# Kernel tuning notes

Hardware: AMD Instinct MI355X
Metric: run time of the kernel (lower is better)

The kernel has to match this reference:

```python
import jax, jax.numpy as jnp
import numpy as np

CUTOFF = 3.0   # self.cutoff
RMIN = 3.5     # rmin in cutoff_function (note rmin > cutoff, faithful to source)
ETA = 4.0
N_RADIAL = 5
N_3BODY = 12
NATOMS = 2048
K = 48         # neighbors per atom (equal counts -> ragged loop becomes dense batch)
HID = 64
NPAIRS = NATOMS * K


def setup_inputs() -> dict:
    key = jax.random.key(0)
    ks = jax.random.split(key, 4)
    # displacements scaled so |rij| is mostly within a few Angstrom
    rij = jax.random.normal(ks[0], (NPAIRS, 3), jnp.float32) * 1.5
    # sorted-by-atom pair list with K neighbors per atom
    unique_i = jnp.repeat(jnp.arange(NATOMS, dtype=jnp.int64), K)
    W1 = jax.random.normal(ks[1], (N_RADIAL + N_3BODY, HID), jnp.float32) * 0.1
    b1 = jnp.zeros((HID,), jnp.float32)
    W2 = jax.random.normal(ks[2], (HID, HID), jnp.float32) * 0.1
    b2 = jnp.zeros((HID,), jnp.float32)
    W3 = jax.random.normal(ks[3], (HID, 1), jnp.float32) * 0.1
    b3 = jnp.zeros((1,), jnp.float32)
    return dict(rij=rij, unique_i=unique_i, W1=W1, b1=b1, W2=W2, b2=b2, W3=W3, b3=b3)


def _energy(rij, W1, b1, W2, b2, W3, b3):
    d = jnp.linalg.norm(rij, axis=1, keepdims=True)           # (P,1)
    diff_norm = rij / jnp.maximum(d, 1e-12)                   # F.normalize
    # pair cutoff (rmin=3.5, c=3.0 as in source)
    fc = jnp.where(d > RMIN,
                   0.5 + 0.5 * jnp.cos(jnp.pi * (d - RMIN) / (CUTOFF - RMIN)),
                   1.0)
    # radial Bessel basis, n = 1..5
    ns = jnp.arange(1, N_RADIAL + 1, dtype=rij.dtype)
    rbf = jnp.sqrt(2.0 / CUTOFF) * jnp.sin(ns * jnp.pi / CUTOFF * d) / d * fc  # (P,5)
    # 3-body Gaussian descriptors
    fcrik = (0.5 + 0.5 * jnp.cos(jnp.pi * d / CUTOFF))[:, 0]  # (P,)
    dn = diff_norm.reshape(NATOMS, K, 3)
    cosang = jnp.einsum('nkd,nld->nkl', dn, dn)               # (N,K,K) pairwise mm
    cosang = jnp.where(jnp.eye(K, dtype=bool)[None], 0.0, cosang)  # fill_diagonal_(0)
    mu = jnp.linspace(-1.0, 1.0, N_3BODY).astype(rij.dtype)
    w = fcrik.reshape(NATOMS, 1, K, 1)                        # fcrik broadcast on axis being summed
    g3b = jnp.sum(jnp.exp(-ETA * (cosang[..., None] - mu) ** 2) * w, axis=2)  # (N,K,12)
    g3b = g3b.reshape(NPAIRS, N_3BODY)
    desc = jnp.concatenate([rbf, g3b], axis=1)                # (P,17)
    h = jnp.tanh(desc @ W1 + b1)
    h = jnp.tanh(h @ W2 + b2)
    eij = h @ W3 + b3                                         # (P,1)
    return jnp.sum(eij * fc)


def reference(rij, unique_i, W1, b1, W2, b2, W3, b3):
    # Module output: gradients of total energy w.r.t. rij (written into beta)
    return jax.grad(_energy)(rij, W1, b1, W2, b2, W3, b3)
```

## Files before the change

kernel.cpp:

```cpp
#include <hip/hip_runtime.h>
#include <hip/hip_bf16.h>

#define NATOMS 2048
#define K 48
#define NR 5
#define NM 12
#define ND 17
#define HID 64

#define PI_F 3.14159265358979f
#define CUT 3.0f
#define RMIN_F 3.5f
#define AFC (-6.28318530717959f)
#define POC (PI_F / CUT)
#define SQ 0.816496580927726f
#define CMC (-0.132231404958678f)
#define N4L (-5.77078016355585f)
#define E1L (2.09846551402031f)
#define TL2 (2.88539008177793f)

__device__ unsigned short g_w1t[64 * 32];
__device__ unsigned short g_w2t[64 * 64];
__device__ unsigned short g_w2r[64 * 64];
__device__ unsigned short g_w1r[32 * 64];

using frag_ab = __attribute__((ext_vector_type(8))) short;
using frag_cd = __attribute__((ext_vector_type(4))) float;
using f2 = __attribute__((ext_vector_type(2))) float;
using f4 = __attribute__((ext_vector_type(4))) float;
using s4 = __attribute__((ext_vector_type(4))) short;

__device__ __forceinline__ float fast_tanh(float x) {
    const float t = __builtin_amdgcn_exp2f(TL2 * x);
    return 1.0f - 2.0f * __builtin_amdgcn_rcpf(t + 1.0f);
}

__device__ __forceinline__ unsigned short f2bs(float x) {
    __hip_bfloat16 b = __float2bfloat16(x);
    return __builtin_bit_cast(unsigned short, b);
}

__device__ __forceinline__ float bs2f(unsigned short u) {
    return __builtin_bit_cast(float, ((unsigned)u) << 16);
}

template <int CTRL>
__device__ __forceinline__ float dpp_add(float x) {
    const int y = __builtin_amdgcn_update_dpp(
        0, __builtin_bit_cast(int, x), CTRL, 0xF, 0xF, true);
    return x + __builtin_bit_cast(float, y);
}

__global__ __launch_bounds__(256) void k_prep(const float* __restrict__ W1,
                                              const float* __restrict__ W2) {
    const int i = blockIdx.x * 256 + threadIdx.x;
    if (i < 2048) {
        const int n = i >> 5, k = i & 31;
        g_w1t[i] = (k < ND) ? f2bs(W1[k * HID + n]) : (unsigned short)0;
    } else if (i < 2048 + 4096) {
        const int j = i - 2048, n = j >> 6, k = j & 63;
        g_w2t[j] = f2bs(W2[k * HID + n]);
    } else if (i < 2048 + 8192) {
        const int j = i - (2048 + 4096);
        g_w2r[j] = f2bs(W2[j]);
    } else if (i < 2048 + 8192 + 2048) {
        const int j = i - (2048 + 8192), n = j >> 6;
        g_w1r[j] = (n < ND) ? f2bs(W1[j]) : (unsigned short)0;
    }
}

#define H1_OFF   0
#define TT_OFF   0
#define SST_OFF  4992
#define GZ2_OFF  6912
#define DESC_OFF 13824
#define SGD_OFF  13824
#define SU_OFF   17664
#define SFC_OFF  18432
#define SFK_OFF  18624
#define SM_BYTES 18816

__global__ __launch_bounds__(64, 2) void k_fused(const float* __restrict__ rij,
                                                 const float* __restrict__ b1,
                                                 const float* __restrict__ b2,
                                                 const float* __restrict__ W3,
                                                 const float* __restrict__ b3,
                                                 float* __restrict__ out) {
    __shared__ __align__(16) char smem[SM_BYTES];
    short*          h1S   = (short*)(smem + H1_OFF);
    unsigned short* tT    = (unsigned short*)(smem + TT_OFF);
    unsigned short* tS    = (unsigned short*)(smem + SST_OFF);
    short*          gz2S  = (short*)(smem + GZ2_OFF);
    short*          descS = (short*)(smem + DESC_OFF);
    float*          sgd   = (float*)(smem + SGD_OFF);
    float*          su    = (float*)(smem + SU_OFF);
    float*          sfc   = (float*)(smem + SFC_OFF);
    float*          sfk   = (float*)(smem + SFK_OFF);

    const int lane = threadIdx.x;
    const int quad = lane >> 4, lm = lane & 15;
    const int base3 = blockIdx.x * (K * 3);

    float b1v[4], b2v[4], w3v[4];
#pragma unroll
    for (int nt = 0; nt < 4; nt++) {
        b1v[nt] = b1[nt * 16 + lm];
        b2v[nt] = b2[nt * 16 + lm];
        w3v[nt] = W3[nt * 16 + lm];
    }
    const float b3v = b3[0];

    if (lane < K) {
        const float x = rij[base3 + 3 * lane];
        const float y = rij[base3 + 3 * lane + 1];
        const float z = rij[base3 + 3 * lane + 2];
        float s2 = fmaxf(x * x + y * y + z * z, 1e-24f);
        const float inv = __builtin_amdgcn_rsqf(s2);
        const float d = s2 * inv;
        *(f4*)&su[4 * lane] = (f4){x * inv, y * inv, z * inv, d};
        sfk[lane] = 0.5f + 0.5f * __cosf(POC * d);
        const float fc = (d > RMIN_F) ? (0.5f + 0.5f * __cosf(AFC * (d - RMIN_F))) : 1.0f;
        sfc[lane] = fc;
        float s1, c1;
        __sincosf(POC * d, &s1, &c1);
        const float sc = SQ * fc * inv;
        float sn = s1, cn = c1;
#pragma unroll 1
        for (int n = 0; n < NR; n++) {
            descS[lane * 40 + n] = (short)f2bs(sc * sn);
            const float snx = sn * c1 + cn * s1;
            cn = cn * c1 - sn * s1;
            sn = snx;
        }
#pragma unroll 1
        for (int c = ND; c < 32; c++) descS[lane * 40 + c] = 0;
    }

    if (lane < K) {
        const int k = lane;
        const f4 uk = *(const f4*)&su[4 * k];
        f2 partv[6];
#pragma unroll
        for (int i = 0; i < 6; i++) partv[i] = (f2){0.0f, 0.0f};
#pragma unroll 1
        for (int l = 0; l < K; l++) {
            const f4 ul = *(const f4*)&su[4 * l];
            float c = uk.x * ul.x + uk.y * ul.y + uk.z * ul.z;
            if (k == l) c = 0.0f;
            const float cp1 = c + 1.0f;
            const float e0 = __builtin_amdgcn_exp2f(N4L * cp1 * cp1) * sfk[l];
            const float e1 = __builtin_amdgcn_exp2f(E1L * cp1);
            const float e2s = e1 * e1;
            const f2 e2v = {e2s, e2s};
            f2 tm = {e0, e0 * e1};
            partv[0] += tm;
#pragma unroll
            for (int i = 1; i < 6; i++) { tm *= e2v; partv[i] += tm; }
        }
#pragma unroll
        for (int i = 0; i < 6; i++) {
            const int m0 = 2 * i, m1 = 2 * i + 1;
            descS[k * 40 + NR + m0] = (short)f2bs(partv[i].x * __expf(CMC * (float)(m0 * m0)));
            descS[k * 40 + NR + m1] = (short)f2bs(partv[i].y * __expf(CMC * (float)(m1 * m1)));
        }
    }

    {
        frag_ab wf1[4];
#pragma unroll
        for (int nt = 0; nt < 4; nt++)
            wf1[nt] = *(const frag_ab*)&g_w1t[(nt * 16 + lm) * 32 + quad * 8];
#pragma unroll 1
        for (int mt = 0; mt < 3; mt++) {
            const frag_ab a = *(const frag_ab*)&descS[(mt * 16 + lm) * 40 + quad * 8];
#pragma unroll
            for (int nt = 0; nt < 4; nt++) {
                frag_cd acc = {b1v[nt], b1v[nt], b1v[nt], b1v[nt]};
                acc = __builtin_amdgcn_mfma_f32_16x16x32_bf16(a, wf1[nt], acc, 0, 0, 0);
#pragma unroll
                for (int r = 0; r < 4; r++)
                    h1S[(mt * 16 + quad * 4 + r) * 72 + nt * 16 + lm] =
                        (short)f2bs(fast_tanh(acc[r]));
            }
        }
    }

    {
        frag_ab wa[4], wb[4];
#pragma unroll
        for (int nt = 0; nt < 4; nt++) {
            wa[nt] = *(const frag_ab*)&g_w2t[(nt * 16 + lm) * 64 + quad * 8];
            wb[nt] = *(const frag_ab*)&g_w2t[(nt * 16 + lm) * 64 + 32 + quad * 8];
        }
#pragma unroll 1
        for (int mt = 0; mt < 3; mt++) {
            const frag_ab a0 = *(const frag_ab*)&h1S[(mt * 16 + lm) * 72 + quad * 8];
            const frag_ab a1 = *(const frag_ab*)&h1S[(mt * 16 + lm) * 72 + 32 + quad * 8];
            const f4 fcv = *(const f4*)&sfc[mt * 16 + quad * 4];
            float ep[4] = {0.0f, 0.0f, 0.0f, 0.0f};
#pragma unroll
            for (int nt = 0; nt < 4; nt++) {
                frag_cd acc = {b2v[nt], b2v[nt], b2v[nt], b2v[nt]};
                acc = __builtin_amdgcn_mfma_f32_16x16x32_bf16(a0, wa[nt], acc, 0, 0, 0);
                acc = __builtin_amdgcn_mfma_f32_16x16x32_bf16(a1, wb[nt], acc, 0, 0, 0);
#pragma unroll
                for (int r = 0; r < 4; r++) {
                    const int row = mt * 16 + quad * 4 + r;
                    const float tv = fast_tanh(acc[r]);
                    ep[r] = fmaf(tv, w3v[nt], ep[r]);
                    gz2S[row * 72 + nt * 16 + lm] =
                        (short)f2bs(fcv[r] * w3v[nt] * (1.0f - tv * tv));
                }
            }
#pragma unroll
            for (int r = 0; r < 4; r++)
                ep[r] = dpp_add<0x118>(dpp_add<0x114>(dpp_add<0x112>(dpp_add<0x111>(ep[r]))));
            if (lm == 15) {
#pragma unroll
                for (int r = 0; r < 4; r++)
                    sgd[(mt * 16 + quad * 4 + r) * 20 + 17] = ep[r] + b3v;
            }
        }
    }

    {
        frag_ab wa[4], wb[4];
#pragma unroll
        for (int nt = 0; nt < 4; nt++) {
            wa[nt] = *(const frag_ab*)&g_w2r[(nt * 16 + lm) * 64 + quad * 8];
            wb[nt] = *(const frag_ab*)&g_w2r[(nt * 16 + lm) * 64 + 32 + quad * 8];
        }
#pragma unroll 1
        for (int mt = 0; mt < 3; mt++) {
            const frag_ab a0 = *(const frag_ab*)&gz2S[(mt * 16 + lm) * 72 + quad * 8];
            const frag_ab a1 = *(const frag_ab*)&gz2S[(mt * 16 + lm) * 72 + 32 + quad * 8];
#pragma unroll
            for (int nt = 0; nt < 4; nt++) {
                frag_cd acc = {0.0f, 0.0f, 0.0f, 0.0f};
                acc = __builtin_amdgcn_mfma_f32_16x16x32_bf16(a0, wa[nt], acc, 0, 0, 0);
                acc = __builtin_amdgcn_mfma_f32_16x16x32_bf16(a1, wb[nt], acc, 0, 0, 0);
#pragma unroll
                for (int r = 0; r < 4; r++) {
                    const int idx = (mt * 16 + quad * 4 + r) * 72 + nt * 16 + lm;
                    const float tv = bs2f((unsigned short)h1S[idx]);
                    h1S[idx] = (short)f2bs(acc[r] * (1.0f - tv * tv));
                }
            }
        }
    }

    {
        frag_ab wa[2], wb[2];
#pragma unroll
        for (int nt = 0; nt < 2; nt++) {
            wa[nt] = *(const frag_ab*)&g_w1r[(nt * 16 + lm) * 64 + quad * 8];
            wb[nt] = *(const frag_ab*)&g_w1r[(nt * 16 + lm) * 64 + 32 + quad * 8];
        }
        const float cm0 = (lm >= NR)
            ? __expf(CMC * (float)((lm - NR) * (lm - NR))) : 1.0f;
        const float cm1 = __expf(-16.0f);
#pragma unroll 1
        for (int mt = 0; mt < 3; mt++) {
            const frag_ab a0 = *(const frag_ab*)&h1S[(mt * 16 + lm) * 72 + quad * 8];
            const frag_ab a1 = *(const frag_ab*)&h1S[(mt * 16 + lm) * 72 + 32 + quad * 8];
            {
                frag_cd acc = {0.0f, 0.0f, 0.0f, 0.0f};
                acc = __builtin_amdgcn_mfma_f32_16x16x32_bf16(a0, wa[0], acc, 0, 0, 0);
                acc = __builtin_amdgcn_mfma_f32_16x16x32_bf16(a1, wb[0], acc, 0, 0, 0);
#pragma unroll
                for (int r = 0; r < 4; r++)
                    sgd[(mt * 16 + quad * 4 + r) * 20 + lm] = acc[r] * cm0;
            }
            {
                frag_cd acc = {0.0f, 0.0f, 0.0f, 0.0f};
                acc = __builtin_amdgcn_mfma_f32_16x16x32_bf16(a0, wa[1], acc, 0, 0, 0);
                acc = __builtin_amdgcn_mfma_f32_16x16x32_bf16(a1, wb[1], acc, 0, 0, 0);
                if (lm == 0) {
#pragma unroll
                    for (int r = 0; r < 4; r++)
                        sgd[(mt * 16 + quad * 4 + r) * 20 + 16] = acc[r] * cm1;
                }
            }
        }
    }

    float gx1 = 0.0f, gy1 = 0.0f, gz1 = 0.0f;
    if (lane < K) {
        const int k = lane;
        f2 gm[NM];
#pragma unroll
        for (int m = 0; m < NM; m++) {
            const float g = sgd[k * 20 + NR + m];
            gm[m] = (f2){g, (float)m * g};
        }
        const f4 uk = *(const f4*)&su[4 * k];
#pragma unroll 1
        for (int l = 0; l < K; l++) {
            const f4 ul = *(const f4*)&su[4 * l];
            float c = uk.x * ul.x + uk.y * ul.y + uk.z * ul.z;
            if (k == l) c = 0.0f;
            const float cp1 = c + 1.0f;
            const float e0 = __builtin_amdgcn_exp2f(N4L * cp1 * cp1);
            const float x = __builtin_amdgcn_exp2f(E1L * cp1);
            const f2 xx = {x, x};
            f2 pd = gm[11];
#pragma unroll
            for (int m = 10; m >= 1; m--) pd = __builtin_elementwise_fma(pd, xx, gm[m]);
            const float Pv = fmaf(pd.x, x, gm[0].x);
            const float T = e0 * Pv;
            const float U = e0 * x * pd.y;
            const float Sp = fmaf(cp1, T, -(2.0f / 11.0f) * U);
            const float Sv = (k == l) ? 0.0f : (-8.0f) * Sp;
            tT[l * 52 + k] = f2bs(T);
            tS[l * 52 + k] = f2bs(Sv);
            const float A = Sv * sfk[l];
            gx1 = fmaf(A, ul.x, gx1);
            gy1 = fmaf(A, ul.y, gy1);
            gz1 = fmaf(A, ul.z, gz1);
        }
    }

    if (lane < K) {
        const int k = lane;
        float sgf_t = 0.0f, gx2 = 0.0f, gy2 = 0.0f, gz2v = 0.0f;
#pragma unroll 1
        for (int i = 0; i < 12; i++) {
            const s4 tv4 = *(const s4*)&tT[k * 52 + 4 * i];
            const s4 sv4 = *(const s4*)&tS[k * 52 + 4 * i];
#pragma unroll
            for (int j = 0; j < 4; j++) {
                const int l = 4 * i + j;
                const f4 ul = *(const f4*)&su[4 * l];
                sgf_t += bs2f((unsigned short)tv4[j]);
                const float Sv = bs2f((unsigned short)sv4[j]);
                gx2 = fmaf(Sv, ul.x, gx2);
                gy2 = fmaf(Sv, ul.y, gy2);
                gz2v = fmaf(Sv, ul.z, gz2v);
            }
        }
        const float fk = sfk[k];
        const float gux = gx1 + fk * gx2;
        const float guy = gy1 + fk * gy2;
        const float guz = gz1 + fk * gz2v;

        const f4 uv = *(const f4*)&su[4 * k];
        const float d = uv.w;
        const float ux = uv.x, uy = uv.y, uz = uv.z;
        const float invd = __builtin_amdgcn_rcpf(d);
        float gfc = sgd[k * 20 + 17];
        float gdR = 0.0f;
        float s1, c1;
        __sincosf(POC * d, &s1, &c1);
        float sn = s1, cn = c1, bn = POC;
#pragma unroll 1
        for (int n = 0; n < NR; n++) {
            const float g = sgd[k * 20 + n];
            gfc = fmaf(g, SQ * sn * invd, gfc);
            gdR = fmaf(g, SQ * (bn * cn - sn * invd) * invd, gdR);
            const float snx = sn * c1 + cn * s1;
            cn = cn * c1 - sn * s1;
            sn = snx;
            bn += POC;
        }
        const float fc = sfc[k];
        float dfc = 0.0f;
        if (d > RMIN_F) dfc = -0.5f * AFC * __sinf(AFC * (d - RMIN_F));
        const float dfcrik = -0.5f * POC * __sinf(POC * d);

        const float gd = fc * gdR + gfc * dfc + sgf_t * dfcrik;
        const float dot = gux * ux + guy * uy + guz * uz;

        out[base3 + 3 * k + 0] = fmaf(gd, ux, (gux - dot * ux) * invd);
        out[base3 + 3 * k + 1] = fmaf(gd, uy, (guy - dot * uy) * invd);
        out[base3 + 3 * k + 2] = fmaf(gd, uz, (guz - dot * uz) * invd);
    }
}

extern "C" void kernel_launch(void* const* d_in, const int* in_sizes, int n_in,
                              void* d_out, int out_size, void* d_ws, size_t ws_size,
                              hipStream_t stream) {
    (void)in_sizes; (void)n_in; (void)out_size; (void)d_ws; (void)ws_size;
    const float* rij = (const float*)d_in[0];
    const float* W1 = (const float*)d_in[2];
    const float* b1 = (const float*)d_in[3];
    const float* W2 = (const float*)d_in[4];
    const float* b2 = (const float*)d_in[5];
    const float* W3 = (const float*)d_in[6];
    const float* b3 = (const float*)d_in[7];
    float* out = (float*)d_out;

    k_prep<<<48, 256, 0, stream>>>(W1, W2);
    k_fused<<<NATOMS, 64, 0, stream>>>(rij, b1, b2, W3, b3, out);
}
```

Baseline: 94.57 us.

## Split each atom across three waves with 4-lane neighbor partitioning

The fused kernel goes from one 64-lane wave per atom to three waves (192 threads), each owning 16 neighbor rows. The pairwise angular loops are split over 4 lanes per row and combined with DPP reductions. The second angular pass now recomputes T and S from the l-side gradient coefficients instead of writing transposed bf16 tiles to shared memory, so shared memory shrinks and more blocks fit per CU. In exchange it repeats the exp and polynomial evaluation, and the early stages rely on wave-local ordering without barriers. That ordering looks fragile: the sgd reads for other rows depend on a single __syncthreads, and su/sfk are written by lanes <48 of every wave, which is redundant but consistent.

After: 100.3 us. 6.1% more time.

```diff
diff --git a/kernel.cpp b/kernel.cpp
--- a/kernel.cpp
+++ b/kernel.cpp
@@ -28,7 +28,6 @@
 using frag_cd = __attribute__((ext_vector_type(4))) float;
 using f2 = __attribute__((ext_vector_type(2))) float;
 using f4 = __attribute__((ext_vector_type(4))) float;
-using s4 = __attribute__((ext_vector_type(4))) short;
 
 __device__ __forceinline__ float fast_tanh(float x) {
     const float t = __builtin_amdgcn_exp2f(TL2 * x);
@@ -69,36 +68,30 @@
     }
 }
 
-#define H1_OFF   0
-#define TT_OFF   0
-#define SST_OFF  4992
-#define GZ2_OFF  6912
-#define DESC_OFF 13824
-#define SGD_OFF  13824
-#define SU_OFF   17664
-#define SFC_OFF  18432
-#define SFK_OFF  18624
-#define SM_BYTES 18816
-
-__global__ __launch_bounds__(64, 2) void k_fused(const float* __restrict__ rij,
-                                                 const float* __restrict__ b1,
-                                                 const float* __restrict__ b2,
-                                                 const float* __restrict__ W3,
-                                                 const float* __restrict__ b3,
-                                                 float* __restrict__ out) {
+#define XS       72
+#define X_OFF    0
+#define SGD_OFF  6912
+#define SU_OFF   10752
+#define SFC_OFF  11520
+#define SFK_OFF  11712
+#define SM_BYTES 11904
+
+__global__ __launch_bounds__(192, 6) void k_fused(const float* __restrict__ rij,
+                                                  const float* __restrict__ b1,
+                                                  const float* __restrict__ b2,
+                                                  const float* __restrict__ W3,
+                                                  const float* __restrict__ b3,
+                                                  float* __restrict__ out) {
     __shared__ __align__(16) char smem[SM_BYTES];
-    short*          h1S   = (short*)(smem + H1_OFF);
-    unsigned short* tT    = (unsigned short*)(smem + TT_OFF);
-    unsigned short* tS    = (unsigned short*)(smem + SST_OFF);
-    short*          gz2S  = (short*)(smem + GZ2_OFF);
-    short*          descS = (short*)(smem + DESC_OFF);
-    float*          sgd   = (float*)(smem + SGD_OFF);
-    float*          su    = (float*)(smem + SU_OFF);
-    float*          sfc   = (float*)(smem + SFC_OFF);
-    float*          sfk   = (float*)(smem + SFK_OFF);
-
-    const int lane = threadIdx.x;
-    const int quad = lane >> 4, lm = lane & 15;
+    short* X   = (short*)(smem + X_OFF);
+    float* sgd = (float*)(smem + SGD_OFF);
+    float* su  = (float*)(smem + SU_OFF);
+    float* sfc = (float*)(smem + SFC_OFF);
+    float* sfk = (float*)(smem + SFK_OFF);
+
+    const int t = threadIdx.x;
+    const int w = t >> 6, lane = t & 63, quad = lane >> 4, lm = lane & 15;
+    const int row0 = 16 * w;
     const int base3 = blockIdx.x * (K * 3);
 
     float b1v[4], b2v[4], w3v[4];
@@ -121,32 +114,36 @@
         sfk[lane] = 0.5f + 0.5f * __cosf(POC * d);
         const float fc = (d > RMIN_F) ? (0.5f + 0.5f * __cosf(AFC * (d - RMIN_F))) : 1.0f;
         sfc[lane] = fc;
-        float s1, c1;
-        __sincosf(POC * d, &s1, &c1);
-        const float sc = SQ * fc * inv;
-        float sn = s1, cn = c1;
-#pragma unroll 1
-        for (int n = 0; n < NR; n++) {
-            descS[lane * 40 + n] = (short)f2bs(sc * sn);
-            const float snx = sn * c1 + cn * s1;
-            cn = cn * c1 - sn * s1;
-            sn = snx;
-        }
-#pragma unroll 1
-        for (int c = ND; c < 32; c++) descS[lane * 40 + c] = 0;
-    }
-
-    if (lane < K) {
-        const int k = lane;
-        const f4 uk = *(const f4*)&su[4 * k];
+        if ((lane >> 4) == w) {
+            float s1, c1;
+            __sincosf(POC * d, &s1, &c1);
+            const float sc = SQ * fc * inv;
+            float sn = s1, cn = c1;
+#pragma unroll 1
+            for (int n = 0; n < NR; n++) {
+                X[lane * XS + n] = (short)f2bs(sc * sn);
+                const float snx = sn * c1 + cn * s1;
+                cn = cn * c1 - sn * s1;
+                sn = snx;
+            }
+#pragma unroll 1
+            for (int c = ND; c < 32; c++) X[lane * XS + c] = 0;
+        }
+    }
+
+    const int r16 = lane >> 2, ch = lane & 3;
+    const int kk = row0 + r16;
+    const f4 ukk = *(const f4*)&su[4 * kk];
+    {
         f2 partv[6];
 #pragma unroll
         for (int i = 0; i < 6; i++) partv[i] = (f2){0.0f, 0.0f};
 #pragma unroll 1
-        for (int l = 0; l < K; l++) {
+        for (int li = 0; li < 12; li++) {
+            const int l = ch * 12 + li;
             const f4 ul = *(const f4*)&su[4 * l];
-            float c = uk.x * ul.x + uk.y * ul.y + uk.z * ul.z;
-            if (k == l) c = 0.0f;
+            float c = ukk.x * ul.x + ukk.y * ul.y + ukk.z * ul.z;
+            if (kk == l) c = 0.0f;
             const float cp1 = c + 1.0f;
             const float e0 = __builtin_amdgcn_exp2f(N4L * cp1 * cp1) * sfk[l];
             const float e1 = __builtin_amdgcn_exp2f(E1L * cp1);
@@ -159,160 +156,145 @@
         }
 #pragma unroll
         for (int i = 0; i < 6; i++) {
-            const int m0 = 2 * i, m1 = 2 * i + 1;
-            descS[k * 40 + NR + m0] = (short)f2bs(partv[i].x * __expf(CMC * (float)(m0 * m0)));
-            descS[k * 40 + NR + m1] = (short)f2bs(partv[i].y * __expf(CMC * (float)(m1 * m1)));
-        }
-    }
-
-    {
-        frag_ab wf1[4];
-#pragma unroll
-        for (int nt = 0; nt < 4; nt++)
-            wf1[nt] = *(const frag_ab*)&g_w1t[(nt * 16 + lm) * 32 + quad * 8];
-#pragma unroll 1
-        for (int mt = 0; mt < 3; mt++) {
-            const frag_ab a = *(const frag_ab*)&descS[(mt * 16 + lm) * 40 + quad * 8];
-#pragma unroll
-            for (int nt = 0; nt < 4; nt++) {
-                frag_cd acc = {b1v[nt], b1v[nt], b1v[nt], b1v[nt]};
-                acc = __builtin_amdgcn_mfma_f32_16x16x32_bf16(a, wf1[nt], acc, 0, 0, 0);
+            partv[i].x = dpp_add<0x4E>(dpp_add<0xB1>(partv[i].x));
+            partv[i].y = dpp_add<0x4E>(dpp_add<0xB1>(partv[i].y));
+        }
+        if (ch == 0) {
+#pragma unroll
+            for (int i = 0; i < 6; i++) {
+                const int m0 = 2 * i, m1 = 2 * i + 1;
+                X[kk * XS + NR + m0] = (short)f2bs(partv[i].x * __expf(CMC * (float)(m0 * m0)));
+                X[kk * XS + NR + m1] = (short)f2bs(partv[i].y * __expf(CMC * (float)(m1 * m1)));
+            }
+        }
+    }
+
+    float t1v[4][4];
+    {
+        const frag_ab a = *(const frag_ab*)&X[(row0 + lm) * XS + quad * 8];
+#pragma unroll
+        for (int nt = 0; nt < 4; nt++) {
+            const frag_ab bfr = *(const frag_ab*)&g_w1t[(nt * 16 + lm) * 32 + quad * 8];
+            frag_cd acc = {b1v[nt], b1v[nt], b1v[nt], b1v[nt]};
+            acc = __builtin_amdgcn_mfma_f32_16x16x32_bf16(a, bfr, acc, 0, 0, 0);
+#pragma unroll
+            for (int r = 0; r < 4; r++) {
+                const float tv = fast_tanh(acc[r]);
+                t1v[nt][r] = tv;
+                X[(row0 + quad * 4 + r) * XS + nt * 16 + lm] = (short)f2bs(tv);
+            }
+        }
+    }
+
+    {
+        const frag_ab a0 = *(const frag_ab*)&X[(row0 + lm) * XS + quad * 8];
+        const frag_ab a1 = *(const frag_ab*)&X[(row0 + lm) * XS + 32 + quad * 8];
+        const f4 fcv = *(const f4*)&sfc[row0 + quad * 4];
+        float ep[4] = {0.0f, 0.0f, 0.0f, 0.0f};
+#pragma unroll
+        for (int nt = 0; nt < 4; nt++) {
+            const frag_ab b0 = *(const frag_ab*)&g_w2t[(nt * 16 + lm) * 64 + quad * 8];
+            const frag_ab b1f = *(const frag_ab*)&g_w2t[(nt * 16 + lm) * 64 + 32 + quad * 8];
+            frag_cd acc = {b2v[nt], b2v[nt], b2v[nt], b2v[nt]};
+            acc = __builtin_amdgcn_mfma_f32_16x16x32_bf16(a0, b0, acc, 0, 0, 0);
+            acc = __builtin_amdgcn_mfma_f32_16x16x32_bf16(a1, b1f, acc, 0, 0, 0);
+#pragma unroll
+            for (int r = 0; r < 4; r++) {
+                const float tv = fast_tanh(acc[r]);
+                ep[r] = fmaf(tv, w3v[nt], ep[r]);
+                X[(row0 + quad * 4 + r) * XS + nt * 16 + lm] =
+                    (short)f2bs(fcv[r] * w3v[nt] * (1.0f - tv * tv));
+            }
+        }
+#pragma unroll
+        for (int r = 0; r < 4; r++)
+            ep[r] = dpp_add<0x118>(dpp_add<0x114>(dpp_add<0x112>(dpp_add<0x111>(ep[r]))));
+        if (lm == 15) {
+#pragma unroll
+            for (int r = 0; r < 4; r++)
+                sgd[(row0 + quad * 4 + r) * 20 + 5] = ep[r] + b3v;
+        }
+    }
+
+    {
+        const frag_ab a0 = *(const frag_ab*)&X[(row0 + lm) * XS + quad * 8];
+        const frag_ab a1 = *(const frag_ab*)&X[(row0 + lm) * XS + 32 + quad * 8];
+#pragma unroll
+        for (int nt = 0; nt < 4; nt++) {
+            const frag_ab b0 = *(const frag_ab*)&g_w2r[(nt * 16 + lm) * 64 + quad * 8];
+            const frag_ab b1f = *(const frag_ab*)&g_w2r[(nt * 16 + lm) * 64 + 32 + quad * 8];
+            frag_cd acc = {0.0f, 0.0f, 0.0f, 0.0f};
+            acc = __builtin_amdgcn_mfma_f32_16x16x32_bf16(a0, b0, acc, 0, 0, 0);
+            acc = __builtin_amdgcn_mfma_f32_16x16x32_bf16(a1, b1f, acc, 0, 0, 0);
+#pragma unroll
+            for (int r = 0; r < 4; r++) {
+                const float g = acc[r] * (1.0f - t1v[nt][r] * t1v[nt][r]);
+                X[(row0 + quad * 4 + r) * XS + nt * 16 + lm] = (short)f2bs(g);
+            }
+        }
+    }
+
+    {
+        const frag_ab a0 = *(const frag_ab*)&X[(row0 + lm) * XS + quad * 8];
+        const frag_ab a1 = *(const frag_ab*)&X[(row0 + lm) * XS + 32 + quad * 8];
+        {
+            const frag_ab b0 = *(const frag_ab*)&g_w1r[lm * 64 + quad * 8];
+            const frag_ab b1f = *(const frag_ab*)&g_w1r[lm * 64 + 32 + quad * 8];
+            frag_cd acc = {0.0f, 0.0f, 0.0f, 0.0f};
+            acc = __builtin_amdgcn_mfma_f32_16x16x32_bf16(a0, b0, acc, 0, 0, 0);
+            acc = __builtin_amdgcn_mfma_f32_16x16x32_bf16(a1, b1f, acc, 0, 0, 0);
+            const int col = (lm < NR) ? lm : lm + 3;
+            const int mm = lm - NR;
+            const float cm = (lm >= NR) ? __expf(CMC * (float)(mm * mm)) : 1.0f;
+#pragma unroll
+            for (int r = 0; r < 4; r++)
+                sgd[(row0 + quad * 4 + r) * 20 + col] = acc[r] * cm;
+        }
+        {
+            const frag_ab b0 = *(const frag_ab*)&g_w1r[(16 + lm) * 64 + quad * 8];
+            const frag_ab b1f = *(const frag_ab*)&g_w1r[(16 + lm) * 64 + 32 + quad * 8];
+            frag_cd acc = {0.0f, 0.0f, 0.0f, 0.0f};
+            acc = __builtin_amdgcn_mfma_f32_16x16x32_bf16(a0, b0, acc, 0, 0, 0);
+            acc = __builtin_amdgcn_mfma_f32_16x16x32_bf16(a1, b1f, acc, 0, 0, 0);
+            if (lm == 0) {
+                const float cm = __expf(-16.0f);
 #pragma unroll
                 for (int r = 0; r < 4; r++)
-                    h1S[(mt * 16 + quad * 4 + r) * 72 + nt * 16 + lm] =
-                        (short)f2bs(fast_tanh(acc[r]));
-            }
-        }
-    }
-
-    {
-        frag_ab wa[4], wb[4];
-#pragma unroll
-        for (int nt = 0; nt < 4; nt++) {
-            wa[nt] = *(const frag_ab*)&g_w2t[(nt * 16 + lm) * 64 + quad * 8];
-            wb[nt] = *(const frag_ab*)&g_w2t[(nt * 16 + lm) * 64 + 32 + quad * 8];
-        }
-#pragma unroll 1
-        for (int mt = 0; mt < 3; mt++) {
-            const frag_ab a0 = *(const frag_ab*)&h1S[(mt * 16 + lm) * 72 + quad * 8];
-            const frag_ab a1 = *(const frag_ab*)&h1S[(mt * 16 + lm) * 72 + 32 + quad * 8];
-            const f4 fcv = *(const f4*)&sfc[mt * 16 + quad * 4];
-            float ep[4] = {0.0f, 0.0f, 0.0f, 0.0f};
-#pragma unroll
-            for (int nt = 0; nt < 4; nt++) {
-                frag_cd acc = {b2v[nt], b2v[nt], b2v[nt], b2v[nt]};
-                acc = __builtin_amdgcn_mfma_f32_16x16x32_bf16(a0, wa[nt], acc, 0, 0, 0);
-                acc = __builtin_amdgcn_mfma_f32_16x16x32_bf16(a1, wb[nt], acc, 0, 0, 0);
-#pragma unroll
-                for (int r = 0; r < 4; r++) {
-                    const int row = mt * 16 + quad * 4 + r;
-                    const float tv = fast_tanh(acc[r]);
-                    ep[r] = fmaf(tv, w3v[nt], ep[r]);
-                    gz2S[row * 72 + nt * 16 + lm] =
-                        (short)f2bs(fcv[r] * w3v[nt] * (1.0f - tv * tv));
-                }
-            }
-#pragma unroll
-            for (int r = 0; r < 4; r++)
-                ep[r] = dpp_add<0x118>(dpp_add<0x114>(dpp_add<0x112>(dpp_add<0x111>(ep[r]))));
-            if (lm == 15) {
-#pragma unroll
-                for (int r = 0; r < 4; r++)
-                    sgd[(mt * 16 + quad * 4 + r) * 20 + 17] = ep[r] + b3v;
-            }
-        }
-    }
-
-    {
-        frag_ab wa[4], wb[4];
-#pragma unroll
-        for (int nt = 0; nt < 4; nt++) {
-            wa[nt] = *(const frag_ab*)&g_w2r[(nt * 16 + lm) * 64 + quad * 8];
-            wb[nt] = *(const frag_ab*)&g_w2r[(nt * 16 + lm) * 64 + 32 + quad * 8];
-        }
-#pragma unroll 1
-        for (int mt = 0; mt < 3; mt++) {
-            const frag_ab a0 = *(const frag_ab*)&gz2S[(mt * 16 + lm) * 72 + quad * 8];
-            const frag_ab a1 = *(const frag_ab*)&gz2S[(mt * 16 + lm) * 72 + 32 + quad * 8];
-#pragma unroll
-            for (int nt = 0; nt < 4; nt++) {
-                frag_cd acc = {0.0f, 0.0f, 0.0f, 0.0f};
-                acc = __builtin_amdgcn_mfma_f32_16x16x32_bf16(a0, wa[nt], acc, 0, 0, 0);
-                acc = __builtin_amdgcn_mfma_f32_16x16x32_bf16(a1, wb[nt], acc, 0, 0, 0);
-#pragma unroll
-                for (int r = 0; r < 4; r++) {
-                    const int idx = (mt * 16 + quad * 4 + r) * 72 + nt * 16 + lm;
-                    const float tv = bs2f((unsigned short)h1S[idx]);
-                    h1S[idx] = (short)f2bs(acc[r] * (1.0f - tv * tv));
-                }
-            }
-        }
-    }
-
-    {
-        frag_ab wa[2], wb[2];
-#pragma unroll
-        for (int nt = 0; nt < 2; nt++) {
-            wa[nt] = *(const frag_ab*)&g_w1r[(nt * 16 + lm) * 64 + quad * 8];
-            wb[nt] = *(const frag_ab*)&g_w1r[(nt * 16 + lm) * 64 + 32 + quad * 8];
-        }
-        const float cm0 = (lm >= NR)
-            ? __expf(CMC * (float)((lm - NR) * (lm - NR))) : 1.0f;
-        const float cm1 = __expf(-16.0f);
-#pragma unroll 1
-        for (int mt = 0; mt < 3; mt++) {
-            const frag_ab a0 = *(const frag_ab*)&h1S[(mt * 16 + lm) * 72 + quad * 8];
-            const frag_ab a1 = *(const frag_ab*)&h1S[(mt * 16 + lm) * 72 + 32 + quad * 8];
-            {
-                frag_cd acc = {0.0f, 0.0f, 0.0f, 0.0f};
-                acc = __builtin_amdgcn_mfma_f32_16x16x32_bf16(a0, wa[0], acc, 0, 0, 0);
-                acc = __builtin_amdgcn_mfma_f32_16x16x32_bf16(a1, wb[0], acc, 0, 0, 0);
-#pragma unroll
-                for (int r = 0; r < 4; r++)
-                    sgd[(mt * 16 + quad * 4 + r) * 20 + lm] = acc[r] * cm0;
-            }
-            {
-                frag_cd acc = {0.0f, 0.0f, 0.0f, 0.0f};
-                acc = __builtin_amdgcn_mfma_f32_16x16x32_bf16(a0, wa[1], acc, 0, 0, 0);
-                acc = __builtin_amdgcn_mfma_f32_16x16x32_bf16(a1, wb[1], acc, 0, 0, 0);
-                if (lm == 0) {
-#pragma unroll
-                    for (int r = 0; r < 4; r++)
-                        sgd[(mt * 16 + quad * 4 + r) * 20 + 16] = acc[r] * cm1;
-                }
+                    sgd[(row0 + quad * 4 + r) * 20 + 19] = acc[r] * cm;
             }
         }
     }
 
     float gx1 = 0.0f, gy1 = 0.0f, gz1 = 0.0f;
-    if (lane < K) {
-        const int k = lane;
-        f2 gm[NM];
-#pragma unroll
-        for (int m = 0; m < NM; m++) {
-            const float g = sgd[k * 20 + NR + m];
-            gm[m] = (f2){g, (float)m * g};
-        }
-        const f4 uk = *(const f4*)&su[4 * k];
-#pragma unroll 1
-        for (int l = 0; l < K; l++) {
+    {
+        const f4 gA = *(const f4*)&sgd[kk * 20 + 8];
+        const f4 gB = *(const f4*)&sgd[kk * 20 + 12];
+        const f4 gC = *(const f4*)&sgd[kk * 20 + 16];
+#pragma unroll 1
+        for (int li = 0; li < 12; li++) {
+            const int l = ch * 12 + li;
             const f4 ul = *(const f4*)&su[4 * l];
-            float c = uk.x * ul.x + uk.y * ul.y + uk.z * ul.z;
-            if (k == l) c = 0.0f;
+            float c = ukk.x * ul.x + ukk.y * ul.y + ukk.z * ul.z;
+            if (kk == l) c = 0.0f;
             const float cp1 = c + 1.0f;
             const float e0 = __builtin_amdgcn_exp2f(N4L * cp1 * cp1);
             const float x = __builtin_amdgcn_exp2f(E1L * cp1);
-            const f2 xx = {x, x};
-            f2 pd = gm[11];
-#pragma unroll
-            for (int m = 10; m >= 1; m--) pd = __builtin_elementwise_fma(pd, xx, gm[m]);
-            const float Pv = fmaf(pd.x, x, gm[0].x);
-            const float T = e0 * Pv;
-            const float U = e0 * x * pd.y;
+            float P = gC[3], Dd = 11.0f * gC[3];
+            P = fmaf(P, x, gC[2]); Dd = fmaf(Dd, x, 10.0f * gC[2]);
+            P = fmaf(P, x, gC[1]); Dd = fmaf(Dd, x, 9.0f * gC[1]);
+            P = fmaf(P, x, gC[0]); Dd = fmaf(Dd, x, 8.0f * gC[0]);
+            P = fmaf(P, x, gB[3]); Dd = fmaf(Dd, x, 7.0f * gB[3]);
+            P = fmaf(P, x, gB[2]); Dd = fmaf(Dd, x, 6.0f * gB[2]);
+            P = fmaf(P, x, gB[1]); Dd = fmaf(Dd, x, 5.0f * gB[1]);
+            P = fmaf(P, x, gB[0]); Dd = fmaf(Dd, x, 4.0f * gB[0]);
+            P = fmaf(P, x, gA[3]); Dd = fmaf(Dd, x, 3.0f * gA[3]);
+            P = fmaf(P, x, gA[2]); Dd = fmaf(Dd, x, 2.0f * gA[2]);
+            P = fmaf(P, x, gA[1]); Dd = fmaf(Dd, x, gA[1]);
+            P = fmaf(P, x, gA[0]);
+            const float T = e0 * P;
+            const float U = e0 * x * Dd;
             const float Sp = fmaf(cp1, T, -(2.0f / 11.0f) * U);
-            const float Sv = (k == l) ? 0.0f : (-8.0f) * Sp;
-            tT[l * 52 + k] = f2bs(T);
-            tS[l * 52 + k] = f2bs(Sv);
+            const float Sv = (kk == l) ? 0.0f : (-8.0f) * Sp;
             const float A = Sv * sfk[l];
             gx1 = fmaf(A, ul.x, gx1);
             gy1 = fmaf(A, ul.y, gy1);
@@ -320,59 +302,87 @@
         }
     }
 
-    if (lane < K) {
-        const int k = lane;
-        float sgf_t = 0.0f, gx2 = 0.0f, gy2 = 0.0f, gz2v = 0.0f;
-#pragma unroll 1
-        for (int i = 0; i < 12; i++) {
-            const s4 tv4 = *(const s4*)&tT[k * 52 + 4 * i];
-            const s4 sv4 = *(const s4*)&tS[k * 52 + 4 * i];
-#pragma unroll
-            for (int j = 0; j < 4; j++) {
-                const int l = 4 * i + j;
-                const f4 ul = *(const f4*)&su[4 * l];
-                sgf_t += bs2f((unsigned short)tv4[j]);
-                const float Sv = bs2f((unsigned short)sv4[j]);
-                gx2 = fmaf(Sv, ul.x, gx2);
-                gy2 = fmaf(Sv, ul.y, gy2);
-                gz2v = fmaf(Sv, ul.z, gz2v);
-            }
-        }
-        const float fk = sfk[k];
-        const float gux = gx1 + fk * gx2;
-        const float guy = gy1 + fk * gy2;
-        const float guz = gz1 + fk * gz2v;
-
-        const f4 uv = *(const f4*)&su[4 * k];
-        const float d = uv.w;
-        const float ux = uv.x, uy = uv.y, uz = uv.z;
-        const float invd = __builtin_amdgcn_rcpf(d);
-        float gfc = sgd[k * 20 + 17];
-        float gdR = 0.0f;
-        float s1, c1;
-        __sincosf(POC * d, &s1, &c1);
-        float sn = s1, cn = c1, bn = POC;
-#pragma unroll 1
-        for (int n = 0; n < NR; n++) {
-            const float g = sgd[k * 20 + n];
-            gfc = fmaf(g, SQ * sn * invd, gfc);
-            gdR = fmaf(g, SQ * (bn * cn - sn * invd) * invd, gdR);
-            const float snx = sn * c1 + cn * s1;
-            cn = cn * c1 - sn * s1;
-            sn = snx;
-            bn += POC;
-        }
-        const float fc = sfc[k];
-        float dfc = 0.0f;
-        if (d > RMIN_F) dfc = -0.5f * AFC * __sinf(AFC * (d - RMIN_F));
-        const float dfcrik = -0.5f * POC * __sinf(POC * d);
-
-        const float gd = fc * gdR + gfc * dfc + sgf_t * dfcrik;
-        const float dot = gux * ux + guy * uy + guz * uz;
-
-        out[base3 + 3 * k + 0] = fmaf(gd, ux, (gux - dot * ux) * invd);
-        out[base3 + 3 * k + 1] = fmaf(gd, uy, (guy - dot * uy) * invd);
-        out[base3 + 3 * k + 2] = fmaf(gd, uz, (guz - dot * uz) * invd);
+    __syncthreads();
+
+    {
+        float sgfp = 0.0f, gx2 = 0.0f, gy2 = 0.0f, gz2p = 0.0f;
+#pragma unroll 1
+        for (int li = 0; li < 12; li++) {
+            const int l = ch * 12 + li;
+            const f4 gA = *(const f4*)&sgd[l * 20 + 8];
+            const f4 gB = *(const f4*)&sgd[l * 20 + 12];
+            const f4 gC = *(const f4*)&sgd[l * 20 + 16];
+            const f4 ul = *(const f4*)&su[4 * l];
+            float c = ukk.x * ul.x + ukk.y * ul.y + ukk.z * ul.z;
+            if (kk == l) c = 0.0f;
+            const float cp1 = c + 1.0f;
+            const float e0 = __builtin_amdgcn_exp2f(N4L * cp1 * cp1);
+            const float x = __builtin_amdgcn_exp2f(E1L * cp1);
+            float P = gC[3], Dd = 11.0f * gC[3];
+            P = fmaf(P, x, gC[2]); Dd = fmaf(Dd, x, 10.0f * gC[2]);
+            P = fmaf(P, x, gC[1]); Dd = fmaf(Dd, x, 9.0f * gC[1]);
+            P = fmaf(P, x, gC[0]); Dd = fmaf(Dd, x, 8.0f * gC[0]);
+            P = fmaf(P, x, gB[3]); Dd = fmaf(Dd, x, 7.0f * gB[3]);
+            P = fmaf(P, x, gB[2]); Dd = fmaf(Dd, x, 6.0f * gB[2]);
+            P = fmaf(P, x, gB[1]); Dd = fmaf(Dd, x, 5.0f * gB[1]);
+            P = fmaf(P, x, gB[0]); Dd = fmaf(Dd, x, 4.0f * gB[0]);
+            P = fmaf(P, x, gA[3]); Dd = fmaf(Dd, x, 3.0f * gA[3]);
+            P = fmaf(P, x, gA[2]); Dd = fmaf(Dd, x, 2.0f * gA[2]);
+            P = fmaf(P, x, gA[1]); Dd = fmaf(Dd, x, gA[1]);
+            P = fmaf(P, x, gA[0]);
+            const float T = e0 * P;
+            const float U = e0 * x * Dd;
+            const float Sp = fmaf(cp1, T, -(2.0f / 11.0f) * U);
+            const float Sv = (kk == l) ? 0.0f : (-8.0f) * Sp;
+            sgfp += T;
+            gx2 = fmaf(Sv, ul.x, gx2);
+            gy2 = fmaf(Sv, ul.y, gy2);
+            gz2p = fmaf(Sv, ul.z, gz2p);
+        }
+        gx1 = dpp_add<0x4E>(dpp_add<0xB1>(gx1));
+        gy1 = dpp_add<0x4E>(dpp_add<0xB1>(gy1));
+        gz1 = dpp_add<0x4E>(dpp_add<0xB1>(gz1));
+        sgfp = dpp_add<0x4E>(dpp_add<0xB1>(sgfp));
+        gx2 = dpp_add<0x4E>(dpp_add<0xB1>(gx2));
+        gy2 = dpp_add<0x4E>(dpp_add<0xB1>(gy2));
+        gz2p = dpp_add<0x4E>(dpp_add<0xB1>(gz2p));
+
+        if (ch == 0) {
+            const float fk = sfk[kk];
+            const float gux = gx1 + fk * gx2;
+            const float guy = gy1 + fk * gy2;
+            const float guz = gz1 + fk * gz2p;
+
+            const float d = ukk.w;
+            const float ux = ukk.x, uy = ukk.y, uz = ukk.z;
+            const float invd = __builtin_amdgcn_rcpf(d);
+            float gfc = sgd[kk * 20 + 5];
+            float gdR = 0.0f;
+            float s1, c1;
+            __sincosf(POC * d, &s1, &c1);
+            float sn = s1, cn = c1, bn = POC;
+#pragma unroll 1
+            for (int n = 0; n < NR; n++) {
+                const float g = sgd[kk * 20 + n];
+                gfc = fmaf(g, SQ * sn * invd, gfc);
+                gdR = fmaf(g, SQ * (bn * cn - sn * invd) * invd, gdR);
+                const float snx = sn * c1 + cn * s1;
+                cn = cn * c1 - sn * s1;
+                sn = snx;
+                bn += POC;
+            }
+            const float fc = sfc[kk];
+            float dfc = 0.0f;
+            if (d > RMIN_F) dfc = -0.5f * AFC * __sinf(AFC * (d - RMIN_F));
+            const float dfcrik = -0.5f * POC * __sinf(POC * d);
+
+            const float gd = fc * gdR + gfc * dfc + sgfp * dfcrik;
+            const float dot = gux * ux + guy * uy + guz * uz;
+
+            out[base3 + 3 * kk + 0] = fmaf(gd, ux, (gux - dot * ux) * invd);
+            out[base3 + 3 * kk + 1] = fmaf(gd, uy, (guy - dot * uy) * invd);
+            out[base3 + 3 * kk + 2] = fmaf(gd, uz, (guz - dot * uz) * invd);
+        }
     }
 }
 
@@ -390,5 +400,5 @@
     float* out = (float*)d_out;
 
     k_prep<<<48, 256, 0, stream>>>(W1, W2);
-    k_fused<<<NATOMS, 64, 0, stream>>>(rij, b1, b2, W3, b3, out);
-}
+    k_fused<<<NATOMS, 192, 0, stream>>>(rij, b1, b2, W3, b3, out);
+}
```
